# Kernel optimization log

Hardware: AMD Instinct MI355X
Metric: run time of the kernel (lower is better)

The kernel has to match this reference:

```python
import jax, jax.numpy as jnp
import numpy as np

K = 16  # knn_graph k, loop=True (self included since d(i,i)=0 is minimal)


def _knn_idx(pos, k):
    # exact kNN via pairwise squared distances; [N, k] neighbor indices
    sq = jnp.sum(pos * pos, axis=-1)
    d2 = sq[:, None] + sq[None, :] - 2.0 * (pos @ pos.T)  # [N, N]
    _, idx = jax.lax.top_k(-d2, k)
    return idx


def _pointnet_conv(x, pos, idx, Wa, ba, Wb, bb):
    # PointNetConv: msg = MLP(concat(x_j, pos_j - pos_i)), max-aggregate over neighbors
    rel = pos[idx] - pos[:, None, :]                    # [N, K, 3]
    m = jnp.concatenate([x[idx], rel], axis=-1)          # [N, K, Cin+3]
    h = jax.nn.relu(m @ Wa + ba) @ Wb + bb               # [N, K, Cout]
    return jnp.max(h, axis=1)                            # [N, Cout]


def setup_inputs() -> dict:
    key = jax.random.key(0)
    ks = jax.random.split(key, 13)
    N = 8192
    c1, c2, c3 = 64, 64, 128
    s = lambda fi: 1.0 / np.sqrt(fi)
    pos = jax.random.normal(ks[0], (N, 3), dtype=jnp.float32)
    return {
        "pos": pos,
        "W1a": jax.random.normal(ks[1], (3 + 3, c1), jnp.float32) * s(6),
        "b1a": jnp.zeros((c1,), jnp.float32),
        "W1b": jax.random.normal(ks[2], (c1, c1), jnp.float32) * s(c1),
        "b1b": jnp.zeros((c1,), jnp.float32),
        "W2a": jax.random.normal(ks[3], (c1 + 3, c2), jnp.float32) * s(c1 + 3),
        "b2a": jnp.zeros((c2,), jnp.float32),
        "W2b": jax.random.normal(ks[4], (c2, c2), jnp.float32) * s(c2),
        "b2b": jnp.zeros((c2,), jnp.float32),
        "W3a": jax.random.normal(ks[5], (c2 + 3, c3), jnp.float32) * s(c2 + 3),
        "b3a": jnp.zeros((c3,), jnp.float32),
        "W3b": jax.random.normal(ks[6], (c3, c3), jnp.float32) * s(c3),
        "b3b": jnp.zeros((c3,), jnp.float32),
    }


def reference(pos, W1a, b1a, W1b, b1b, W2a, b2a, W2b, b2b, W3a, b3a, W3b, b3b):
    idx = _knn_idx(pos, K)
    h1 = jax.nn.relu(_pointnet_conv(pos, pos, idx, W1a, b1a, W1b, b1b))
    h2 = jax.nn.relu(_pointnet_conv(h1, pos, idx, W2a, b2a, W2b, b2b))
    h3 = jax.nn.relu(_pointnet_conv(h2, pos, idx, W3a, b3a, W3b, b3b))
    return (h1, h2, h3)
```

## Files before the change

kernel.cpp:

```cpp
#include <hip/hip_runtime.h>
#include <math.h>

#define N_PTS 8192
#define KNN 16

typedef __attribute__((ext_vector_type(8))) short bf16x8;
typedef __attribute__((ext_vector_type(4))) float f32x4v;

__device__ __forceinline__ unsigned short f2bf(float f)
{
    unsigned u = __float_as_uint(f);
    u = u + 0x7fffu + ((u >> 16) & 1u);
    return (unsigned short)(u >> 16);
}
__device__ __forceinline__ unsigned pack2(float a, float b)
{
    return (unsigned)f2bf(a) | ((unsigned)f2bf(b) << 16);
}
__device__ __forceinline__ float rfl(float x)
{
    return __int_as_float(__builtin_amdgcn_readfirstlane(__float_as_int(x)));
}
__device__ __forceinline__ unsigned short bfup(float f)
{
    const unsigned u = __float_as_uint(f);
    return (unsigned short)((u >> 31) ? (u >> 16) : ((u + 0xFFFFu) >> 16));
}
__device__ __forceinline__ float bfex(unsigned short h)
{
    return __uint_as_float((unsigned)h << 16);
}

__global__ __launch_bounds__(256) void prep_all(
    const float* __restrict__ pos, float4* __restrict__ pos4,
    const float* __restrict__ w1a, const float* __restrict__ w1b,
    const float* __restrict__ w2a, const float* __restrict__ w2b,
    const float* __restrict__ w3a, const float* __restrict__ w3b,
    uint4* __restrict__ dst)
{
    const int b = blockIdx.x;
    if (b < 88) {
        if (threadIdx.x >= 64) return;
        const float* Ws[6] = {w1a, w1b, w2a, w2b, w3a, w3b};
        const int Kd[6] = {6, 64, 67, 64, 67, 128};
        const int Nd[6] = {64, 64, 64, 64, 128, 128};
        const int start[7] = {0, 4, 12, 24, 32, 56, 88};
        int m = 0;
        while (b >= start[m + 1]) ++m;
        const int f  = b - start[m];
        const int NT = Nd[m] / 16;
        const int ks = f / NT, nt = f % NT;
        const int lane = threadIdx.x;
        const int c  = nt * 16 + (lane & 15);
        const int k0 = ks * 32 + (lane >> 4) * 8;
        const int K = Kd[m], N = Nd[m];
        const float* W = Ws[m];
        float v[8];
#pragma unroll
        for (int j = 0; j < 8; ++j) {
            const int kk = k0 + j;
            v[j] = (kk < K) ? W[kk * N + c] : 0.0f;
        }
        uint4 o;
        o.x = pack2(v[0], v[1]); o.y = pack2(v[2], v[3]);
        o.z = pack2(v[4], v[5]); o.w = pack2(v[6], v[7]);
        dst[b * 64 + lane] = o;
    } else {
        const int i = (b - 88) * 256 + threadIdx.x;
        const float x = pos[i * 3 + 0];
        const float y = pos[i * 3 + 1];
        const float z = pos[i * 3 + 2];
        pos4[i] = make_float4(x, y, z, fmaf(x, x, fmaf(y, y, z * z)));
    }
}

__device__ __forceinline__ unsigned sortkey(const float d2)
{
    unsigned u = __float_as_uint(d2);
    u ^= (unsigned)((int)u >> 31) | 0x80000000u;
    return u;
}

constexpr int CAP   = 128;
constexpr int QB    = 8;
constexpr int NWV   = 8;
constexpr int TILE  = 512;
constexpr int NTL   = N_PTS / TILE;

__device__ __forceinline__ void stage_tile(const float4* src, float4* dst)
{
    __builtin_amdgcn_global_load_lds(
        (const __attribute__((address_space(1))) void*)src,
        (__attribute__((address_space(3))) void*)dst, 16, 0, 0);
}

__global__ __launch_bounds__(512, 8) void knn_kernel(const float4* __restrict__ pos4,
                                                     int* __restrict__ idx_out)
{
    __shared__ float4 tile[2][TILE];
    __shared__ unsigned short minsbf[QB][NWV][64];
    __shared__ float Ts[QB];
    __shared__ unsigned long long surv[QB][CAP];
    __shared__ int scnt[QB];

    const int tid   = threadIdx.x;
    const int w     = tid >> 6;
    const int lane  = tid & 63;
    const int qbase = blockIdx.x * QB;

    if (tid < QB) scnt[tid] = 0;

    float qx[QB], qy[QB], qz[QB];
#pragma unroll
    for (int qi = 0; qi < QB; ++qi) {
        const float4 qp = pos4[qbase + qi];
        qx[qi] = rfl(-2.0f * qp.x);
        qy[qi] = rfl(-2.0f * qp.y);
        qz[qi] = rfl(-2.0f * qp.z);
    }

    const float4* src = pos4 + w * 64 + lane;

    float mn[QB];
#pragma unroll
    for (int qi = 0; qi < QB; ++qi) mn[qi] = 1e30f;

    stage_tile(src, &tile[0][w * 64]);
    __syncthreads();
#pragma unroll 1
    for (int t = 0; t < NTL; ++t) {
        if (t + 1 < NTL)
            stage_tile(src + (t + 1) * TILE, &tile[(t + 1) & 1][w * 64]);
        const float4 p = tile[t & 1][w * 64 + lane];
#pragma unroll
        for (int qi = 0; qi < QB; ++qi) {
            const float s = fmaf(qx[qi], p.x, fmaf(qy[qi], p.y, fmaf(qz[qi], p.z, p.w)));
            mn[qi] = fminf(mn[qi], s);
        }
        __syncthreads();
    }
#pragma unroll
    for (int qi = 0; qi < QB; ++qi) minsbf[qi][w][lane] = bfup(mn[qi]);
    __syncthreads();

    {
        const int q = w;
        float v = bfex(minsbf[q][0][lane]);
#pragma unroll
        for (int k = 1; k < NWV; ++k) v = fminf(v, bfex(minsbf[q][k][lane]));
#pragma unroll
        for (int kk = 2; kk <= 64; kk <<= 1)
#pragma unroll
            for (int j = kk >> 1; j > 0; j >>= 1) {
                const float o = __shfl_xor(v, j);
                const bool up = ((lane & kk) == 0);
                const bool lo = ((lane & j) == 0);
                v = (up == lo) ? fminf(v, o) : fmaxf(v, o);
            }
        if (lane == 15) Ts[q] = v;
    }
    __syncthreads();

    float T[QB];
#pragma unroll
    for (int qi = 0; qi < QB; ++qi) T[qi] = rfl(Ts[qi]);

    stage_tile(src, &tile[0][w * 64]);
    __syncthreads();
#pragma unroll 1
    for (int t = 0; t < NTL; ++t) {
        if (t + 1 < NTL)
            stage_tile(src + (t + 1) * TILE, &tile[(t + 1) & 1][w * 64]);
        const float4 p = tile[t & 1][w * 64 + lane];
        const int j = t * TILE + w * 64 + lane;
#pragma unroll
        for (int qi = 0; qi < QB; ++qi) {
            const float s = fmaf(qx[qi], p.x, fmaf(qy[qi], p.y, fmaf(qz[qi], p.z, p.w)));
            if (s <= T[qi]) {
                const int slot = atomicAdd(&scnt[qi], 1);
                if (slot < CAP)
                    surv[qi][slot] = ((unsigned long long)sortkey(s) << 32) | (unsigned)j;
            }
        }
        __syncthreads();
    }

    {
        const int q = w;
        const int n = min(scnt[q], CAP);
        const unsigned long long k0 = (lane < n) ? surv[q][lane] : ~0ull;
        const unsigned long long k1 = (lane + 64 < n) ? surv[q][lane + 64] : ~0ull;
        int r0 = 0, r1 = 0;
#pragma unroll 4
        for (int e = 0; e < n; ++e) {
            const unsigned long long ke = surv[q][e];
            r0 += (ke < k0) ? 1 : 0;
            r1 += (ke < k1) ? 1 : 0;
        }
        if (lane < n && r0 < KNN)
            idx_out[(qbase + q) * KNN + r0] = (int)(unsigned)(k0 & 0xFFFFFFFFu);
        if (lane + 64 < n && r1 < KNN)
            idx_out[(qbase + q) * KNN + r1] = (int)(unsigned)(k1 & 0xFFFFFFFFu);
    }
}

template <int CIN, int CMID, int COUT, int WM, int WN>
__global__ __launch_bounds__(256) void conv_mfma(
    const float* __restrict__ x, const float* __restrict__ pos,
    const int* __restrict__ idx,
    const uint4* __restrict__ fA, const float* __restrict__ ba,
    const uint4* __restrict__ fB, const float* __restrict__ bb,
    float* __restrict__ out)
{
    constexpr int PB  = 8, M = 128;
    constexpr int K1  = (CIN + 3 + 31) & ~31;
    constexpr int KS1 = K1 / 32;
    constexpr int KP1 = K1 + 8;
    constexpr int KS2 = CMID / 32;
    constexpr int KP2 = CMID + 8;
    constexpr int NT  = COUT / 16;
    constexpr int NTW = NT / WN;
    constexpr int MFW = (M / 16) / WM;
    constexpr int MSGS = M * KP1;
    constexpr int HBS  = M * KP2;
    constexpr int BUFS = (MSGS > HBS) ? MSGS : HBS;

    __shared__ int nbr[M];
    __shared__ __align__(16) unsigned short buf[BUFS];

    const int tid  = threadIdx.x;
    const int lane = tid & 63;
    const int w    = tid >> 6;
    const int wm   = w / WN, wn = w % WN;
    const int i0   = blockIdx.x * PB;

    if (tid < M) nbr[tid] = idx[i0 * KNN + tid];
    __syncthreads();

    if constexpr (CIN == 3) {
        if (tid < M) {
            const int row = tid, p = row >> 4, j = nbr[row];
            const float ax = pos[j * 3 + 0], ay = pos[j * 3 + 1], az = pos[j * 3 + 2];
            const float bx = pos[(i0 + p) * 3 + 0], by = pos[(i0 + p) * 3 + 1],
                        bz = pos[(i0 + p) * 3 + 2];
            uint4 c0;
            c0.x = pack2(ax, ay);
            c0.y = pack2(az, ax - bx);
            c0.z = pack2(ay - by, az - bz);
            c0.w = 0u;
            *reinterpret_cast<uint4*>(&buf[row * KP1 + 0])  = c0;
            const uint4 z = make_uint4(0, 0, 0, 0);
            *reinterpret_cast<uint4*>(&buf[row * KP1 + 8])  = z;
            *reinterpret_cast<uint4*>(&buf[row * KP1 + 16]) = z;
            *reinterpret_cast<uint4*>(&buf[row * KP1 + 24]) = z;
        }
    } else {
        const int row = tid >> 1, hh = tid & 1;
        const int j = nbr[row];
        const float* xr = x + j * CIN + hh * 32;
#pragma unroll
        for (int cc = 0; cc < 32; cc += 8) {
            const float4 f0 = *reinterpret_cast<const float4*>(xr + cc);
            const float4 f1 = *reinterpret_cast<const float4*>(xr + cc + 4);
            uint4 o;
            o.x = pack2(f0.x, f0.y); o.y = pack2(f0.z, f0.w);
            o.z = pack2(f1.x, f1.y); o.w = pack2(f1.z, f1.w);
            *reinterpret_cast<uint4*>(&buf[row * KP1 + hh * 32 + cc]) = o;
        }
        if (hh) {
            const int p = row >> 4;
            const float rx = pos[j * 3 + 0] - pos[(i0 + p) * 3 + 0];
            const float ry = pos[j * 3 + 1] - pos[(i0 + p) * 3 + 1];
            const float rz = pos[j * 3 + 2] - pos[(i0 + p) * 3 + 2];
            uint4 c0;
            c0.x = pack2(rx, ry);
            c0.y = pack2(rz, 0.0f);
            c0.z = 0u; c0.w = 0u;
            *reinterpret_cast<uint4*>(&buf[row * KP1 + 64]) = c0;
            const uint4 z = make_uint4(0, 0, 0, 0);
            *reinterpret_cast<uint4*>(&buf[row * KP1 + 72]) = z;
            *reinterpret_cast<uint4*>(&buf[row * KP1 + 80]) = z;
            *reinterpret_cast<uint4*>(&buf[row * KP1 + 88]) = z;
        }
    }
    __syncthreads();

    f32x4v acc[MFW][NTW];
    {
        uint4 b1[KS1][NTW];
#pragma unroll
        for (int ks = 0; ks < KS1; ++ks)
#pragma unroll
            for (int nt = 0; nt < NTW; ++nt)
                b1[ks][nt] = fA[(ks * NT + wn * NTW + nt) * 64 + lane];

#pragma unroll
        for (int mf = 0; mf < MFW; ++mf)
#pragma unroll
            for (int nt = 0; nt < NTW; ++nt) acc[mf][nt] = (f32x4v)0.0f;

#pragma unroll
        for (int mf = 0; mf < MFW; ++mf) {
            bf16x8 a[KS1];
#pragma unroll
            for (int ks = 0; ks < KS1; ++ks)
                a[ks] = *reinterpret_cast<const bf16x8*>(
                    &buf[((wm * MFW + mf) * 16 + (lane & 15)) * KP1 + ks * 32 + (lane >> 4) * 8]);
#pragma unroll
            for (int nt = 0; nt < NTW; ++nt)
#pragma unroll
                for (int ks = 0; ks < KS1; ++ks)
                    acc[mf][nt] = __builtin_amdgcn_mfma_f32_16x16x32_bf16(
                        a[ks], __builtin_bit_cast(bf16x8, b1[ks][nt]), acc[mf][nt], 0, 0, 0);
        }
    }
    __syncthreads();

    {
        float bav[NTW];
#pragma unroll
        for (int nt = 0; nt < NTW; ++nt) bav[nt] = ba[(wn * NTW + nt) * 16 + (lane & 15)];
#pragma unroll
        for (int mf = 0; mf < MFW; ++mf)
#pragma unroll
            for (int nt = 0; nt < NTW; ++nt)
#pragma unroll
                for (int r = 0; r < 4; ++r) {
                    const float v = fmaxf(acc[mf][nt][r] + bav[nt], 0.0f);
                    buf[((wm * MFW + mf) * 16 + (lane >> 4) * 4 + r) * KP2 +
                        (wn * NTW + nt) * 16 + (lane & 15)] = f2bf(v);
                }
    }
    __syncthreads();

    {
        uint4 b2[KS2][NTW];
#pragma unroll
        for (int ks = 0; ks < KS2; ++ks)
#pragma unroll
            for (int nt = 0; nt < NTW; ++nt)
                b2[ks][nt] = fB[(ks * NT + wn * NTW + nt) * 64 + lane];

        f32x4v acc2[MFW][NTW];
#pragma unroll
        for (int mf = 0; mf < MFW; ++mf)
#pragma unroll
            for (int nt = 0; nt < NTW; ++nt) acc2[mf][nt] = (f32x4v)0.0f;

#pragma unroll
        for (int mf = 0; mf < MFW; ++mf) {
            bf16x8 a[KS2];
#pragma unroll
            for (int ks = 0; ks < KS2; ++ks)
                a[ks] = *reinterpret_cast<const bf16x8*>(
                    &buf[((wm * MFW + mf) * 16 + (lane & 15)) * KP2 + ks * 32 + (lane >> 4) * 8]);
#pragma unroll
            for (int nt = 0; nt < NTW; ++nt)
#pragma unroll
                for (int ks = 0; ks < KS2; ++ks)
                    acc2[mf][nt] = __builtin_amdgcn_mfma_f32_16x16x32_bf16(
                        a[ks], __builtin_bit_cast(bf16x8, b2[ks][nt]), acc2[mf][nt], 0, 0, 0);
        }

        float bbv[NTW];
#pragma unroll
        for (int nt = 0; nt < NTW; ++nt) bbv[nt] = bb[(wn * NTW + nt) * 16 + (lane & 15)];

#pragma unroll
        for (int mf = 0; mf < MFW; ++mf)
#pragma unroll
            for (int nt = 0; nt < NTW; ++nt) {
                const f32x4v t = acc2[mf][nt];
                float m0 = fmaxf(fmaxf(t[0], t[1]), fmaxf(t[2], t[3]));
                m0 = fmaxf(m0, __shfl_xor(m0, 16));
                m0 = fmaxf(m0, __shfl_xor(m0, 32));
                const float v = fmaxf(m0 + bbv[nt], 0.0f);
                if (lane < 16)
                    out[(i0 + wm * MFW + mf) * COUT + (wn * NTW + nt) * 16 + lane] = v;
            }
    }
}

extern "C" void kernel_launch(void* const* d_in, const int* in_sizes, int n_in,
                              void* d_out, int out_size, void* d_ws, size_t ws_size,
                              hipStream_t stream)
{
    const float* pos = (const float*)d_in[0];
    const float* W1a = (const float*)d_in[1];
    const float* b1a = (const float*)d_in[2];
    const float* W1b = (const float*)d_in[3];
    const float* b1b = (const float*)d_in[4];
    const float* W2a = (const float*)d_in[5];
    const float* b2a = (const float*)d_in[6];
    const float* W2b = (const float*)d_in[7];
    const float* b2b = (const float*)d_in[8];
    const float* W3a = (const float*)d_in[9];
    const float* b3a = (const float*)d_in[10];
    const float* W3b = (const float*)d_in[11];
    const float* b3b = (const float*)d_in[12];

    float* out = (float*)d_out;
    float* h1 = out;
    float* h2 = out + N_PTS * 64;
    float* h3 = out + N_PTS * 128;

    int*   idx     = (int*)d_ws;
    uint4* wsFrags = (uint4*)((char*)d_ws + N_PTS * KNN * 4);

    float4* pos4 = (float4*)h3;

    prep_all<<<120, 256, 0, stream>>>(pos, pos4, W1a, W1b, W2a, W2b, W3a, W3b, wsFrags);
    knn_kernel<<<N_PTS / QB, 512, 0, stream>>>(pos4, idx);

    const uint4* fW1a = wsFrags + 0 * 64;
    const uint4* fW1b = wsFrags + 4 * 64;
    const uint4* fW2a = wsFrags + 12 * 64;
    const uint4* fW2b = wsFrags + 24 * 64;
    const uint4* fW3a = wsFrags + 32 * 64;
    const uint4* fW3b = wsFrags + 56 * 64;

    conv_mfma<3, 64, 64, 4, 1><<<N_PTS / 8, 256, 0, stream>>>(
        pos, pos, idx, fW1a, b1a, fW1b, b1b, h1);
    conv_mfma<64, 64, 64, 4, 1><<<N_PTS / 8, 256, 0, stream>>>(
        h1, pos, idx, fW2a, b2a, fW2b, b2b, h2);
    conv_mfma<64, 128, 128, 2, 2><<<N_PTS / 8, 256, 0, stream>>>(
        h2, pos, idx, fW3a, b3a, fW3b, b3b, h3);
}
```

Measured before the change: 76.93 us.

## Process 16 queries per kNN block and reduce column minima with LDS atomicMin

```diff
diff --git a/kernel.cpp b/kernel.cpp
--- a/kernel.cpp
+++ b/kernel.cpp
@@ -20,15 +20,6 @@
 __device__ __forceinline__ float rfl(float x)
 {
     return __int_as_float(__builtin_amdgcn_readfirstlane(__float_as_int(x)));
-}
-__device__ __forceinline__ unsigned short bfup(float f)
-{
-    const unsigned u = __float_as_uint(f);
-    return (unsigned short)((u >> 31) ? (u >> 16) : ((u + 0xFFFFu) >> 16));
-}
-__device__ __forceinline__ float bfex(unsigned short h)
-{
-    return __uint_as_float((unsigned)h << 16);
 }
 
 __global__ __launch_bounds__(256) void prep_all(
@@ -80,11 +71,15 @@
     u ^= (unsigned)((int)u >> 31) | 0x80000000u;
     return u;
 }
+__device__ __forceinline__ float unkey(unsigned k)
+{
+    const unsigned u = (k & 0x80000000u) ? (k ^ 0x80000000u) : ~k;
+    return __uint_as_float(u);
+}
 
 constexpr int CAP   = 128;
-constexpr int QB    = 8;
-constexpr int NWV   = 8;
-constexpr int TILE  = 512;
+constexpr int QB    = 16;
+constexpr int TILE  = 1024;
 constexpr int NTL   = N_PTS / TILE;
 
 __device__ __forceinline__ void stage_tile(const float4* src, float4* dst)
@@ -94,11 +89,11 @@
         (__attribute__((address_space(3))) void*)dst, 16, 0, 0);
 }
 
-__global__ __launch_bounds__(512, 8) void knn_kernel(const float4* __restrict__ pos4,
-                                                     int* __restrict__ idx_out)
+__global__ __launch_bounds__(512) void knn_kernel(const float4* __restrict__ pos4,
+                                                  int* __restrict__ idx_out)
 {
     __shared__ float4 tile[2][TILE];
-    __shared__ unsigned short minsbf[QB][NWV][64];
+    __shared__ unsigned minkey[QB][64];
     __shared__ float Ts[QB];
     __shared__ unsigned long long surv[QB][CAP];
     __shared__ int scnt[QB];
@@ -109,6 +104,8 @@
     const int qbase = blockIdx.x * QB;
 
     if (tid < QB) scnt[tid] = 0;
+    reinterpret_cast<unsigned*>(minkey)[tid]       = 0xFFFFFFFFu;
+    reinterpret_cast<unsigned*>(minkey)[tid + 512] = 0xFFFFFFFFu;
 
     float qx[QB], qy[QB], qz[QB];
 #pragma unroll
@@ -119,45 +116,49 @@
         qz[qi] = rfl(-2.0f * qp.z);
     }
 
-    const float4* src = pos4 + w * 64 + lane;
+    const float4* src = pos4 + w * 128 + lane;
 
     float mn[QB];
 #pragma unroll
     for (int qi = 0; qi < QB; ++qi) mn[qi] = 1e30f;
 
-    stage_tile(src, &tile[0][w * 64]);
+    stage_tile(src,      &tile[0][w * 128]);
+    stage_tile(src + 64, &tile[0][w * 128 + 64]);
     __syncthreads();
 #pragma unroll 1
     for (int t = 0; t < NTL; ++t) {
-        if (t + 1 < NTL)
-            stage_tile(src + (t + 1) * TILE, &tile[(t + 1) & 1][w * 64]);
-        const float4 p = tile[t & 1][w * 64 + lane];
+        if (t + 1 < NTL) {
+            stage_tile(src + (t + 1) * TILE,      &tile[(t + 1) & 1][w * 128]);
+            stage_tile(src + (t + 1) * TILE + 64, &tile[(t + 1) & 1][w * 128 + 64]);
+        }
+        const float4 p0 = tile[t & 1][w * 128 + lane];
+        const float4 p1 = tile[t & 1][w * 128 + 64 + lane];
 #pragma unroll
         for (int qi = 0; qi < QB; ++qi) {
-            const float s = fmaf(qx[qi], p.x, fmaf(qy[qi], p.y, fmaf(qz[qi], p.z, p.w)));
-            mn[qi] = fminf(mn[qi], s);
+            const float s0 = fmaf(qx[qi], p0.x, fmaf(qy[qi], p0.y, fmaf(qz[qi], p0.z, p0.w)));
+            const float s1 = fmaf(qx[qi], p1.x, fmaf(qy[qi], p1.y, fmaf(qz[qi], p1.z, p1.w)));
+            mn[qi] = fminf(mn[qi], fminf(s0, s1));
         }
         __syncthreads();
     }
 #pragma unroll
-    for (int qi = 0; qi < QB; ++qi) minsbf[qi][w][lane] = bfup(mn[qi]);
-    __syncthreads();
-
-    {
-        const int q = w;
-        float v = bfex(minsbf[q][0][lane]);
-#pragma unroll
-        for (int k = 1; k < NWV; ++k) v = fminf(v, bfex(minsbf[q][k][lane]));
+    for (int qi = 0; qi < QB; ++qi) atomicMin(&minkey[qi][lane], sortkey(mn[qi]));
+    __syncthreads();
+
+#pragma unroll
+    for (int k = 0; k < 2; ++k) {
+        const int q = w * 2 + k;
+        unsigned v = minkey[q][lane];
 #pragma unroll
         for (int kk = 2; kk <= 64; kk <<= 1)
 #pragma unroll
             for (int j = kk >> 1; j > 0; j >>= 1) {
-                const float o = __shfl_xor(v, j);
+                const unsigned o = __shfl_xor(v, j);
                 const bool up = ((lane & kk) == 0);
                 const bool lo = ((lane & j) == 0);
-                v = (up == lo) ? fminf(v, o) : fmaxf(v, o);
+                v = (up == lo) ? min(v, o) : max(v, o);
             }
-        if (lane == 15) Ts[q] = v;
+        if (lane == 15) Ts[q] = unkey(v);
     }
     __syncthreads();
 
@@ -165,28 +166,35 @@
 #pragma unroll
     for (int qi = 0; qi < QB; ++qi) T[qi] = rfl(Ts[qi]);
 
-    stage_tile(src, &tile[0][w * 64]);
+    stage_tile(src,      &tile[0][w * 128]);
+    stage_tile(src + 64, &tile[0][w * 128 + 64]);
     __syncthreads();
 #pragma unroll 1
     for (int t = 0; t < NTL; ++t) {
-        if (t + 1 < NTL)
-            stage_tile(src + (t + 1) * TILE, &tile[(t + 1) & 1][w * 64]);
-        const float4 p = tile[t & 1][w * 64 + lane];
-        const int j = t * TILE + w * 64 + lane;
-#pragma unroll
-        for (int qi = 0; qi < QB; ++qi) {
-            const float s = fmaf(qx[qi], p.x, fmaf(qy[qi], p.y, fmaf(qz[qi], p.z, p.w)));
-            if (s <= T[qi]) {
-                const int slot = atomicAdd(&scnt[qi], 1);
-                if (slot < CAP)
-                    surv[qi][slot] = ((unsigned long long)sortkey(s) << 32) | (unsigned)j;
+        if (t + 1 < NTL) {
+            stage_tile(src + (t + 1) * TILE,      &tile[(t + 1) & 1][w * 128]);
+            stage_tile(src + (t + 1) * TILE + 64, &tile[(t + 1) & 1][w * 128 + 64]);
+        }
+#pragma unroll
+        for (int u = 0; u < 2; ++u) {
+            const float4 p = tile[t & 1][w * 128 + u * 64 + lane];
+            const int j = t * TILE + w * 128 + u * 64 + lane;
+#pragma unroll
+            for (int qi = 0; qi < QB; ++qi) {
+                const float s = fmaf(qx[qi], p.x, fmaf(qy[qi], p.y, fmaf(qz[qi], p.z, p.w)));
+                if (s <= T[qi]) {
+                    const int slot = atomicAdd(&scnt[qi], 1);
+                    if (slot < CAP)
+                        surv[qi][slot] = ((unsigned long long)sortkey(s) << 32) | (unsigned)j;
+                }
             }
         }
         __syncthreads();
     }
 
-    {
-        const int q = w;
+#pragma unroll
+    for (int k = 0; k < 2; ++k) {
+        const int q = w * 2 + k;
         const int n = min(scnt[q], CAP);
         const unsigned long long k0 = (lane < n) ? surv[q][lane] : ~0ull;
         const unsigned long long k1 = (lane + 64 < n) ? surv[q][lane + 64] : ~0ull;
```

Result: no change. 76.90 us (-0.0%).
